# Optimization experiments

Hardware: AMD Instinct MI355X
Metric: run time of the kernel (lower is better)

The kernel has to match this reference:

```python
import jax, jax.numpy as jnp
import numpy as np

N = 50000
E = 800000
D = 128
LN_EPS = 1e-5


def setup_inputs() -> dict:
    key = jax.random.key(0)
    ks = jax.random.split(key, 12)
    s = 1.0 / np.sqrt(D)
    return {
        "x": jax.random.normal(ks[0], (N, D), dtype=jnp.float32),
        "edge_index": jax.random.randint(ks[1], (2, E), 0, N, dtype=jnp.int64),
        "edge_attr": jax.random.normal(ks[2], (E, D), dtype=jnp.float32),
        # GINEConv edge projection Linear(edge_dim=D, in_channels=D)
        "Wl": jax.random.uniform(ks[3], (D, D), jnp.float32, -s, s),
        "bl": jax.random.uniform(ks[4], (D,), jnp.float32, -s, s),
        # mlp: Linear(D,D) -> ReLU -> Linear(D,D)
        "W1": jax.random.uniform(ks[5], (D, D), jnp.float32, -s, s),
        "b1": jax.random.uniform(ks[6], (D,), jnp.float32, -s, s),
        "W2": jax.random.uniform(ks[7], (D, D), jnp.float32, -s, s),
        "b2": jax.random.uniform(ks[8], (D,), jnp.float32, -s, s),
        # PyG LayerNorm affine
        "ln_w": jnp.ones((D,), jnp.float32),
        "ln_b": jnp.zeros((D,), jnp.float32),
    }


def reference(x, edge_index, edge_attr, Wl, bl, W1, b1, W2, b2, ln_w, ln_b):
    src = edge_index[0]  # j (message source)
    dst = edge_index[1]  # i (aggregation target)
    # GINEConv message: ReLU(x_j + lin(edge_attr)) -- gather + elementwise
    e = edge_attr @ Wl + bl                      # [E, D]
    msg = jax.nn.relu(x[src] + e)                # [E, D]
    # scatter-sum aggregation into destination nodes
    agg = jax.ops.segment_sum(msg, dst, num_segments=N)  # [N, D]
    # eps = 0 (train_eps=False): nn((1+eps)*x + agg)
    h = x + agg
    h = jax.nn.relu(h @ W1 + b1) @ W2 + b2       # MLP
    # residual
    h = h + x
    # PyG LayerNorm, mode='graph', batch=None: normalize over all entries
    mu = jnp.mean(h)
    std = jnp.sqrt(jnp.mean((h - mu) ** 2))
    h = (h - mu) / (std + LN_EPS) * ln_w + ln_b
    # SiLU, dropout(eval)=identity, nan_to_num
    h = jax.nn.silu(h)
    return jnp.nan_to_num(h)
```

## Files before the change

kernel.cpp:

```cpp
#include <hip/hip_runtime.h>
#include <math.h>

#define NN 50000
#define EE 800000
#define D128 128
#define LN_EPSF 1e-5f

#define NBK 12500
#define CAP 128

typedef __bf16 bf16_t;
typedef __bf16 bf16x8 __attribute__((ext_vector_type(8)));
typedef float f32x4 __attribute__((ext_vector_type(4)));

#define AGG_F (NN * D128)

__device__ __forceinline__ bf16x8 cvt8(float4 f0, float4 f1) {
    bf16x8 r;
    r[0] = (bf16_t)f0.x; r[1] = (bf16_t)f0.y; r[2] = (bf16_t)f0.z; r[3] = (bf16_t)f0.w;
    r[4] = (bf16_t)f1.x; r[5] = (bf16_t)f1.y; r[6] = (bf16_t)f1.z; r[7] = (bf16_t)f1.w;
    return r;
}

__device__ __forceinline__ bf16x8 zero8() {
    bf16x8 z;
    #pragma unroll
    for (int j = 0; j < 8; ++j) z[j] = (bf16_t)0.f;
    return z;
}

__device__ __forceinline__ void load_w_lds(const float* __restrict__ W, bf16_t* Wlds,
                                           const float* __restrict__ bias, float* b_s) {
    int tid = threadIdx.x;
    for (int i = tid; i < D128 * D128; i += 256) {
        int k = i >> 7, n = i & 127;
        Wlds[(n * D128 + k) ^ ((n & 7) << 3)] = (bf16_t)W[i];
    }
    if (tid < D128) b_s[tid] = bias[tid];
    __syncthreads();
}

__global__ __launch_bounds__(256) void k_zero0(int* __restrict__ cursor,
                                               float* __restrict__ sc,
                                               const int* __restrict__ ei32,
                                               int* __restrict__ flag) {
    const int idx = blockIdx.x * 256 + threadIdx.x;
    if (blockIdx.x == 0 && threadIdx.x < 64) {
        unsigned long long m = __ballot(ei32[2 * threadIdx.x + 1] == 0);
        if (threadIdx.x == 0) { flag[0] = (m == ~0ULL) ? 1 : 0; sc[0] = 0.f; sc[1] = 0.f; }
    }
    for (int i = idx; i < NBK; i += gridDim.x * 256) cursor[i] = 0;
}

__device__ __forceinline__ void idx_pair(const void* ei, int is64, int e, int& sj, int& di) {
    if (is64) {
        const long long* p = (const long long*)ei;
        sj = (int)p[e]; di = (int)p[EE + e];
    } else {
        const int* p = (const int*)ei;
        sj = p[e]; di = p[EE + e];
    }
}

__global__ __launch_bounds__(256) void k_scatter(const void* __restrict__ eidx,
                                                 const int* __restrict__ flag,
                                                 int* __restrict__ cursor,
                                                 int2* __restrict__ entries) {
    const int is64 = flag[0];
    for (int e = blockIdx.x * 256 + threadIdx.x; e < EE; e += gridDim.x * 256) {
        int sj, di;
        idx_pair(eidx, is64, e, sj, di);
        const int b = di >> 2;
        const int dl = di & 3;
        const int p = atomicAdd(&cursor[b], 1);
        if (p < CAP) entries[(size_t)b * CAP + p] = make_int2(e, (dl << 16) | sj);
    }
}

__global__ __launch_bounds__(256) void k_bagg(
    const float* __restrict__ ea, const float* __restrict__ x,
    const float* __restrict__ Wl, const float* __restrict__ bl,
    const int2* __restrict__ entries, const int* __restrict__ cursor,
    float* __restrict__ agg)
{
    __shared__ bf16_t Wlds[D128 * D128];
    __shared__ float bl_s[D128];
    load_w_lds(Wl, Wlds, bl, bl_s);

    const int lane = threadIdx.x & 63, wid = threadIdx.x >> 6;
    const int l15 = lane & 15, lg = lane >> 4;
    const int b = blockIdx.x * 4 + wid;

    float blv[8];
    #pragma unroll
    for (int q = 0; q < 8; ++q) blv[q] = bl_s[l15 + 16 * q];

    const int2* eb = entries + (size_t)b * CAP;
    const int cnt = min(cursor[b], CAP);
    const int ntiles = (cnt + 15) >> 4;

    float ns0[8], ns1[8], ns2[8], ns3[8];
    #pragma unroll
    for (int q = 0; q < 8; ++q) { ns0[q] = 0.f; ns1[q] = 0.f; ns2[q] = 0.f; ns3[q] = 0.f; }

    for (int t = 0; t < ntiles; ++t) {
        const int p = t * 16 + l15;
        const int2 en = (p < cnt) ? eb[p] : make_int2(0, 0);
        const int eid = en.x;

        int yr[4];
        #pragma unroll
        for (int i = 0; i < 4; ++i) yr[i] = __shfl(en.y, lg * 4 + i, 16);

        float xv[4][8];
        #pragma unroll
        for (int i = 0; i < 4; ++i) {
            const float* xr = x + (size_t)(yr[i] & 0xffff) * D128;
            #pragma unroll
            for (int q = 0; q < 8; ++q) xv[i][q] = xr[l15 + 16 * q];
        }

        bf16x8 a[4];
        {
            const float* rp = ea + (size_t)eid * D128 + lg * 8;
            #pragma unroll
            for (int s = 0; s < 4; ++s) {
                float4 f0 = *(const float4*)(rp + s * 32);
                float4 f1 = *(const float4*)(rp + s * 32 + 4);
                a[s] = cvt8(f0, f1);
            }
        }

        f32x4 acc[8];
        #pragma unroll
        for (int q = 0; q < 8; ++q) acc[q] = f32x4{0.f, 0.f, 0.f, 0.f};
        #pragma unroll
        for (int s = 0; s < 4; ++s) {
            const int kb = s * 32 + lg * 8;
            #pragma unroll
            for (int q = 0; q < 8; ++q) {
                const int col = l15 + 16 * q;
                bf16x8 bf = *(const bf16x8*)&Wlds[(col * D128 + kb) ^ ((col & 7) << 3)];
                acc[q] = __builtin_amdgcn_mfma_f32_16x16x32_bf16(a[s], bf, acc[q], 0, 0, 0);
            }
        }

        #pragma unroll
        for (int i = 0; i < 4; ++i) {
            const int r = lg * 4 + i;
            const bool vr = (t * 16 + r) < cnt;
            const int dl_r = (yr[i] >> 16) & 3;
            #pragma unroll
            for (int q = 0; q < 8; ++q) {
                float v = fmaxf(acc[q][i] + blv[q] + xv[i][q], 0.f);
                v = vr ? v : 0.f;
                ns0[q] += (dl_r == 0) ? v : 0.f;
                ns1[q] += (dl_r == 1) ? v : 0.f;
                ns2[q] += (dl_r == 2) ? v : 0.f;
                ns3[q] += (dl_r == 3) ? v : 0.f;
            }
        }
    }

    #pragma unroll
    for (int q = 0; q < 8; ++q) {
        ns0[q] += __shfl_xor(ns0[q], 16); ns0[q] += __shfl_xor(ns0[q], 32);
        ns1[q] += __shfl_xor(ns1[q], 16); ns1[q] += __shfl_xor(ns1[q], 32);
        ns2[q] += __shfl_xor(ns2[q], 16); ns2[q] += __shfl_xor(ns2[q], 32);
        ns3[q] += __shfl_xor(ns3[q], 16); ns3[q] += __shfl_xor(ns3[q], 32);
    }
    float* ag = agg + (size_t)(b * 4 + lg) * D128 + l15;
    if (lg == 0) {
        #pragma unroll
        for (int q = 0; q < 8; ++q) ag[16 * q] = ns0[q];
    } else if (lg == 1) {
        #pragma unroll
        for (int q = 0; q < 8; ++q) ag[16 * q] = ns1[q];
    } else if (lg == 2) {
        #pragma unroll
        for (int q = 0; q < 8; ++q) ag[16 * q] = ns2[q];
    } else {
        #pragma unroll
        for (int q = 0; q < 8; ++q) ag[16 * q] = ns3[q];
    }
}

__global__ __launch_bounds__(256) void k_mlp1(
    const float* __restrict__ x, const float* __restrict__ agg,
    const float* __restrict__ W1, const float* __restrict__ b1,
    float* __restrict__ tbuf)
{
    __shared__ bf16_t Wlds[D128 * D128];
    __shared__ float b_s[D128];
    load_w_lds(W1, Wlds, b1, b_s);

    const int lane = threadIdx.x & 63, wid = threadIdx.x >> 6;
    const int l15 = lane & 15, lg = lane >> 4;
    const int nbase = blockIdx.x * 64 + wid * 16;
    if (nbase >= NN) return;

    const int row = nbase + l15;
    bf16x8 a[4];
    if (row < NN) {
        const float* xr = x + (size_t)row * D128 + lg * 8;
        const float* gr = agg + (size_t)row * D128 + lg * 8;
        #pragma unroll
        for (int s = 0; s < 4; ++s) {
            float4 f0 = *(const float4*)(xr + s * 32);
            float4 f1 = *(const float4*)(xr + s * 32 + 4);
            float4 g0 = *(const float4*)(gr + s * 32);
            float4 g1 = *(const float4*)(gr + s * 32 + 4);
            float4 h0 = {f0.x + g0.x, f0.y + g0.y, f0.z + g0.z, f0.w + g0.w};
            float4 h1 = {f1.x + g1.x, f1.y + g1.y, f1.z + g1.z, f1.w + g1.w};
            a[s] = cvt8(h0, h1);
        }
    } else {
        #pragma unroll
        for (int s = 0; s < 4; ++s) a[s] = zero8();
    }
    f32x4 acc[8];
    #pragma unroll
    for (int t = 0; t < 8; ++t) acc[t] = f32x4{0.f, 0.f, 0.f, 0.f};
    #pragma unroll
    for (int s = 0; s < 4; ++s) {
        const int kb = s * 32 + lg * 8;
        #pragma unroll
        for (int t = 0; t < 8; ++t) {
            const int col = l15 + 16 * t;
            bf16x8 b = *(const bf16x8*)&Wlds[(col * D128 + kb) ^ ((col & 7) << 3)];
            acc[t] = __builtin_amdgcn_mfma_f32_16x16x32_bf16(a[s], b, acc[t], 0, 0, 0);
        }
    }
    #pragma unroll
    for (int i = 0; i < 4; ++i) {
        const int r = nbase + lg * 4 + i;
        if (r < NN) {
            float* tr = tbuf + (size_t)r * D128;
            #pragma unroll
            for (int t = 0; t < 8; ++t) {
                const int c = l15 + 16 * t;
                tr[c] = fmaxf(acc[t][i] + b_s[c], 0.0f);
            }
        }
    }
}

__global__ __launch_bounds__(256) void k_mlp2(
    const float* __restrict__ tbuf, const float* __restrict__ x,
    const float* __restrict__ W2, const float* __restrict__ b2,
    float* __restrict__ out, float* __restrict__ sc)
{
    __shared__ bf16_t Wlds[D128 * D128];
    __shared__ float b_s[D128];
    __shared__ float red[8];
    load_w_lds(W2, Wlds, b2, b_s);

    const int tid = threadIdx.x;
    const int lane = tid & 63, wid = tid >> 6;
    const int l15 = lane & 15, lg = lane >> 4;
    const int nbase = blockIdx.x * 64 + wid * 16;
    float s1 = 0.f, s2 = 0.f;

    if (nbase < NN) {
        const int row = nbase + l15;
        bf16x8 a[4];
        if (row < NN) {
            const float* rp = tbuf + (size_t)row * D128 + lg * 8;
            #pragma unroll
            for (int s = 0; s < 4; ++s) {
                float4 f0 = *(const float4*)(rp + s * 32);
                float4 f1 = *(const float4*)(rp + s * 32 + 4);
                a[s] = cvt8(f0, f1);
            }
        } else {
            #pragma unroll
            for (int s = 0; s < 4; ++s) a[s] = zero8();
        }
        f32x4 acc[8];
        #pragma unroll
        for (int t = 0; t < 8; ++t) acc[t] = f32x4{0.f, 0.f, 0.f, 0.f};
        #pragma unroll
        for (int s = 0; s < 4; ++s) {
            const int kb = s * 32 + lg * 8;
            #pragma unroll
            for (int t = 0; t < 8; ++t) {
                const int col = l15 + 16 * t;
                bf16x8 b = *(const bf16x8*)&Wlds[(col * D128 + kb) ^ ((col & 7) << 3)];
                acc[t] = __builtin_amdgcn_mfma_f32_16x16x32_bf16(a[s], b, acc[t], 0, 0, 0);
            }
        }
        #pragma unroll
        for (int i = 0; i < 4; ++i) {
            const int r = nbase + lg * 4 + i;
            if (r < NN) {
                #pragma unroll
                for (int t = 0; t < 8; ++t) {
                    const int c = l15 + 16 * t;
                    float v = acc[t][i] + b_s[c] + x[(size_t)r * D128 + c];
                    out[(size_t)r * D128 + c] = v;
                    s1 += v;
                    s2 += v * v;
                }
            }
        }
    }
    #pragma unroll
    for (int o = 32; o > 0; o >>= 1) {
        s1 += __shfl_xor(s1, o);
        s2 += __shfl_xor(s2, o);
    }
    if (lane == 0) { red[wid * 2] = s1; red[wid * 2 + 1] = s2; }
    __syncthreads();
    if (tid == 0) {
        float a1 = red[0] + red[2] + red[4] + red[6];
        float a2 = red[1] + red[3] + red[5] + red[7];
        unsafeAtomicAdd(&sc[0], a1);
        unsafeAtomicAdd(&sc[1], a2);
    }
}

__global__ __launch_bounds__(256) void k_ln(
    float* __restrict__ out, const float* __restrict__ sc,
    const float* __restrict__ lnw, const float* __restrict__ lnb)
{
    const float inv = 1.0f / (float)(NN * D128);
    const float mu = sc[0] * inv;
    const float var = sc[1] * inv - mu * mu;
    const float rstd = 1.0f / (sqrtf(fmaxf(var, 0.f)) + LN_EPSF);
    const int total = NN * D128 / 4;
    for (int idx = blockIdx.x * 256 + threadIdx.x; idx < total; idx += gridDim.x * 256) {
        float4 h = ((const float4*)out)[idx];
        const int c0 = (idx * 4) & 127;
        float4 w = *(const float4*)(lnw + c0);
        float4 bb = *(const float4*)(lnb + c0);
        float4 r;
        r.x = (h.x - mu) * rstd * w.x + bb.x;
        r.y = (h.y - mu) * rstd * w.y + bb.y;
        r.z = (h.z - mu) * rstd * w.z + bb.z;
        r.w = (h.w - mu) * rstd * w.w + bb.w;
        r.x = r.x / (1.f + __expf(-r.x));
        r.y = r.y / (1.f + __expf(-r.y));
        r.z = r.z / (1.f + __expf(-r.z));
        r.w = r.w / (1.f + __expf(-r.w));
        if (r.x != r.x) r.x = 0.f;
        if (r.y != r.y) r.y = 0.f;
        if (r.z != r.z) r.z = 0.f;
        if (r.w != r.w) r.w = 0.f;
        ((float4*)out)[idx] = r;
    }
}

extern "C" void kernel_launch(void* const* d_in, const int* in_sizes, int n_in,
                              void* d_out, int out_size, void* d_ws, size_t ws_size,
                              hipStream_t stream)
{
    const float* x   = (const float*)d_in[0];
    const void*  ei  = d_in[1];
    const float* ea  = (const float*)d_in[2];
    const float* Wl  = (const float*)d_in[3];
    const float* bl  = (const float*)d_in[4];
    const float* W1  = (const float*)d_in[5];
    const float* b1  = (const float*)d_in[6];
    const float* W2  = (const float*)d_in[7];
    const float* b2  = (const float*)d_in[8];
    const float* lnw = (const float*)d_in[9];
    const float* lnb = (const float*)d_in[10];
    float* out = (float*)d_out;

    float* agg = (float*)d_ws;
    float* sc  = agg + AGG_F;
    int* flag  = (int*)(sc + 2);

    int2* entries = (int2*)d_out;
    int* cursor   = (int*)(entries + (size_t)NBK * CAP);

    k_zero0<<<49, 256, 0, stream>>>(cursor, sc, (const int*)ei, flag);
    k_scatter<<<1024, 256, 0, stream>>>(ei, flag, cursor, entries);
    k_bagg<<<NBK / 4, 256, 0, stream>>>(ea, x, Wl, bl, entries, cursor, agg);
    k_mlp1<<<(NN + 63) / 64, 256, 0, stream>>>(x, agg, W1, b1, out);
    k_mlp2<<<(NN + 63) / 64, 256, 0, stream>>>(out, x, W2, b2, out, sc);
    k_ln<<<NN * D128 / 4 / 256, 256, 0, stream>>>(out, sc, lnw, lnb);
}
```

Before: 393.2 us.

## Gather x rows as float4 and add them via identity MFMA; preload edge entries

Each lane now fetches its bucket's edge entries once into registers and broadcasts them per tile with shuffles, instead of loading from global memory every tile. The source-node row x_j is loaded with vectorized float4 reads in the same layout as the edge_attr A-operand. It is converted to bf16 and added into the accumulator through two extra MFMAs against identity B-fragments. This replaces 32 strided scalar loads per lane per tile. The cost is two extra MFMAs per k-step, and x_j is now rounded to bf16, which loosens accuracy.

```diff
diff --git a/kernel.cpp b/kernel.cpp
--- a/kernel.cpp
+++ b/kernel.cpp
@@ -91,12 +91,23 @@
     const int l15 = lane & 15, lg = lane >> 4;
     const int b = blockIdx.x * 4 + wid;
 
+    bf16x8 id0 = zero8(), id1 = zero8();
+    #pragma unroll
+    for (int j = 0; j < 8; ++j) {
+        if (8 * lg + j == l15)      id0[j] = (bf16_t)1.0f;
+        if (8 * lg + j == l15 + 16) id1[j] = (bf16_t)1.0f;
+    }
     float blv[8];
     #pragma unroll
     for (int q = 0; q < 8; ++q) blv[q] = bl_s[l15 + 16 * q];
 
     const int2* eb = entries + (size_t)b * CAP;
     const int cnt = min(cursor[b], CAP);
+    int2 m0 = eb[lane];
+    int2 m1 = eb[64 + lane];
+    if (lane >= cnt)      m0 = make_int2(0, 0);
+    if (64 + lane >= cnt) m1 = make_int2(0, 0);
+
     const int ntiles = (cnt + 15) >> 4;
 
     float ns0[8], ns1[8], ns2[8], ns3[8];
@@ -104,30 +115,30 @@
     for (int q = 0; q < 8; ++q) { ns0[q] = 0.f; ns1[q] = 0.f; ns2[q] = 0.f; ns3[q] = 0.f; }
 
     for (int t = 0; t < ntiles; ++t) {
-        const int p = t * 16 + l15;
-        const int2 en = (p < cnt) ? eb[p] : make_int2(0, 0);
-        const int eid = en.x;
-
-        int yr[4];
-        #pragma unroll
-        for (int i = 0; i < 4; ++i) yr[i] = __shfl(en.y, lg * 4 + i, 16);
-
-        float xv[4][8];
-        #pragma unroll
-        for (int i = 0; i < 4; ++i) {
-            const float* xr = x + (size_t)(yr[i] & 0xffff) * D128;
-            #pragma unroll
-            for (int q = 0; q < 8; ++q) xv[i][q] = xr[l15 + 16 * q];
-        }
-
-        bf16x8 a[4];
+        const int sl = (t * 16 + l15) & 63;
+        const bool lo = (t < 4);
+        const int ex = lo ? __shfl(m0.x, sl) : __shfl(m1.x, sl);
+        const int ey = lo ? __shfl(m0.y, sl) : __shfl(m1.y, sl);
+        const int eid = ex;
+        const int src = ey & 0xffff;
+
+        int dlr[4];
+        #pragma unroll
+        for (int i = 0; i < 4; ++i) dlr[i] = (__shfl(ey, lg * 4 + i, 16) >> 16) & 3;
+
+        float4 eF[8], xF[8];
         {
             const float* rp = ea + (size_t)eid * D128 + lg * 8;
             #pragma unroll
             for (int s = 0; s < 4; ++s) {
-                float4 f0 = *(const float4*)(rp + s * 32);
-                float4 f1 = *(const float4*)(rp + s * 32 + 4);
-                a[s] = cvt8(f0, f1);
+                eF[2 * s]     = *(const float4*)(rp + s * 32);
+                eF[2 * s + 1] = *(const float4*)(rp + s * 32 + 4);
+            }
+            const float* xp = x + (size_t)src * D128 + lg * 8;
+            #pragma unroll
+            for (int s = 0; s < 4; ++s) {
+                xF[2 * s]     = *(const float4*)(xp + s * 32);
+                xF[2 * s + 1] = *(const float4*)(xp + s * 32 + 4);
             }
         }
 
@@ -136,28 +147,30 @@
         for (int q = 0; q < 8; ++q) acc[q] = f32x4{0.f, 0.f, 0.f, 0.f};
         #pragma unroll
         for (int s = 0; s < 4; ++s) {
+            const bf16x8 af = cvt8(eF[2 * s], eF[2 * s + 1]);
             const int kb = s * 32 + lg * 8;
             #pragma unroll
             for (int q = 0; q < 8; ++q) {
                 const int col = l15 + 16 * q;
                 bf16x8 bf = *(const bf16x8*)&Wlds[(col * D128 + kb) ^ ((col & 7) << 3)];
-                acc[q] = __builtin_amdgcn_mfma_f32_16x16x32_bf16(a[s], bf, acc[q], 0, 0, 0);
-            }
+                acc[q] = __builtin_amdgcn_mfma_f32_16x16x32_bf16(af, bf, acc[q], 0, 0, 0);
+            }
+            const bf16x8 xf = cvt8(xF[2 * s], xF[2 * s + 1]);
+            acc[2 * s]     = __builtin_amdgcn_mfma_f32_16x16x32_bf16(xf, id0, acc[2 * s], 0, 0, 0);
+            acc[2 * s + 1] = __builtin_amdgcn_mfma_f32_16x16x32_bf16(xf, id1, acc[2 * s + 1], 0, 0, 0);
         }
 
         #pragma unroll
         for (int i = 0; i < 4; ++i) {
-            const int r = lg * 4 + i;
-            const bool vr = (t * 16 + r) < cnt;
-            const int dl_r = (yr[i] >> 16) & 3;
+            const bool vr = (t * 16 + lg * 4 + i) < cnt;
             #pragma unroll
             for (int q = 0; q < 8; ++q) {
-                float v = fmaxf(acc[q][i] + blv[q] + xv[i][q], 0.f);
+                float v = fmaxf(acc[q][i] + blv[q], 0.f);
                 v = vr ? v : 0.f;
-                ns0[q] += (dl_r == 0) ? v : 0.f;
-                ns1[q] += (dl_r == 1) ? v : 0.f;
-                ns2[q] += (dl_r == 2) ? v : 0.f;
-                ns3[q] += (dl_r == 3) ? v : 0.f;
+                ns0[q] += (dlr[i] == 0) ? v : 0.f;
+                ns1[q] += (dlr[i] == 1) ? v : 0.f;
+                ns2[q] += (dlr[i] == 2) ? v : 0.f;
+                ns3[q] += (dlr[i] == 3) ? v : 0.f;
             }
         }
     }
```

New measurement: 406.8 us. +3.5%, slower.
